# Performance work log

Hardware: AMD Instinct MI355X
Metric: run time of the kernel (lower is better)

## Reference

```python
import jax, jax.numpy as jnp
import numpy as np

HIDDEN = 2048
N_HEADS = 16
N_KV_HEADS = 8
HEAD_DIM = 128
ROTARY_DIM = 32  # int(128 * 0.25), already even
ROPE_THETA = 10000000.0
EPS = 1e-6
BATCH, SEQ = 2, 2048


def _rmsnorm(x, w, eps=EPS):
    # per-head RMSNorm over last dim; weight is zero-init, scale = 1 + w
    r = jax.lax.rsqrt(jnp.mean(x * x, axis=-1, keepdims=True) + eps)
    return x * r * (1.0 + w)


def _rope(x, positions, rotary_dim, theta):
    # x: [b, s, h, rotary_dim]; rotate-halves RoPE
    half = rotary_dim // 2
    inv_freq = 1.0 / (theta ** (jnp.arange(half, dtype=jnp.float32) / half))
    ang = positions.astype(jnp.float32)[:, :, None] * inv_freq  # [b, s, half]
    cos = jnp.cos(ang)[:, :, None, :]
    sin = jnp.sin(ang)[:, :, None, :]
    x1, x2 = x[..., :half], x[..., half:]
    return jnp.concatenate([x1 * cos - x2 * sin, x1 * sin + x2 * cos], axis=-1)


def setup_inputs() -> dict:
    key = jax.random.key(0)
    ks = jax.random.split(key, 8)
    scale = lambda fan_in: 1.0 / np.sqrt(fan_in)
    x = jax.random.normal(ks[0], (BATCH, SEQ, HIDDEN), dtype=jnp.float32)
    Wq = jax.random.normal(ks[1], (HIDDEN, N_HEADS * HEAD_DIM * 2), jnp.float32) * scale(HIDDEN)
    Wk = jax.random.normal(ks[2], (HIDDEN, N_KV_HEADS * HEAD_DIM), jnp.float32) * scale(HIDDEN)
    Wv = jax.random.normal(ks[3], (HIDDEN, N_KV_HEADS * HEAD_DIM), jnp.float32) * scale(HIDDEN)
    Wo = jax.random.normal(ks[4], (N_HEADS * HEAD_DIM, HIDDEN), jnp.float32) * scale(N_HEADS * HEAD_DIM)
    q_norm_w = jax.random.normal(ks[5], (HEAD_DIM,), jnp.float32) * 0.02
    k_norm_w = jax.random.normal(ks[6], (HEAD_DIM,), jnp.float32) * 0.02
    attention_mask = jnp.ones((BATCH, SEQ), dtype=jnp.int32)
    positions = jnp.broadcast_to(jnp.arange(SEQ, dtype=jnp.int32), (BATCH, SEQ))
    return {"x": x, "attention_mask": attention_mask, "positions": positions,
            "Wq": Wq, "Wk": Wk, "Wv": Wv, "Wo": Wo,
            "q_norm_w": q_norm_w, "k_norm_w": k_norm_w}


def reference(x, attention_mask, positions, Wq, Wk, Wv, Wo, q_norm_w, k_norm_w):
    b, s, _ = x.shape
    g = N_HEADS // N_KV_HEADS  # GQA group size

    q_all = jnp.einsum('bsh,ho->bso', x, Wq).reshape(b, s, N_HEADS, HEAD_DIM * 2)
    q, gate = jnp.split(q_all, 2, axis=-1)          # each [b,s,H,D]
    gate = gate.reshape(b, s, N_HEADS * HEAD_DIM)
    q = _rmsnorm(q, q_norm_w)
    k = _rmsnorm(jnp.einsum('bsh,ho->bso', x, Wk).reshape(b, s, N_KV_HEADS, HEAD_DIM), k_norm_w)
    v = jnp.einsum('bsh,ho->bso', x, Wv).reshape(b, s, N_KV_HEADS, HEAD_DIM)

    # partial RoPE on first ROTARY_DIM dims
    q = jnp.concatenate([_rope(q[..., :ROTARY_DIM], positions, ROTARY_DIM, ROPE_THETA), q[..., ROTARY_DIM:]], axis=-1)
    k = jnp.concatenate([_rope(k[..., :ROTARY_DIM], positions, ROTARY_DIM, ROPE_THETA), k[..., ROTARY_DIM:]], axis=-1)

    # grouped-query causal attention
    qg = q.reshape(b, s, N_KV_HEADS, g, HEAD_DIM)
    scores = jnp.einsum('bqhgd,bkhd->bhgqk', qg, k) / jnp.sqrt(jnp.float32(HEAD_DIM))
    causal = jnp.tril(jnp.ones((s, s), dtype=bool))
    key_valid = attention_mask.astype(bool)[:, None, None, None, :]  # [b,1,1,1,k]
    mask = causal[None, None, None, :, :] & key_valid
    scores = jnp.where(mask, scores, jnp.finfo(scores.dtype).min)
    probs = jax.nn.softmax(scores, axis=-1)
    attn = jnp.einsum('bhgqk,bkhd->bqhgd', probs, v).reshape(b, s, N_HEADS * HEAD_DIM)

    attn = attn * jax.nn.sigmoid(gate)
    return jnp.einsum('bso,oh->bsh', attn, Wo)
```

## Files before the change

### kernel.cpp

```cpp
#include <hip/hip_runtime.h>
#include <cstdint>

typedef __bf16  bf16;
typedef __bf16  bf16x8 __attribute__((ext_vector_type(8)));
typedef __bf16  bf16x4 __attribute__((ext_vector_type(4)));
typedef __bf16  bf16x2 __attribute__((ext_vector_type(2)));
typedef float   f32x4  __attribute__((ext_vector_type(4)));
typedef float   f32x16 __attribute__((ext_vector_type(16)));

#define GLOAD_LDS16(g, l) __builtin_amdgcn_global_load_lds( \
    (const __attribute__((address_space(1))) void*)(g),     \
    (__attribute__((address_space(3))) void*)(l), 16, 0, 0)

#define SEQ   2048
#define HID   2048
#define NH    16
#define NKV   8
#define HD    128
#define NQKV  6144
#define MTOT  4096

__device__ __forceinline__ void transw_body(const float* __restrict__ W, bf16* __restrict__ WT,
                                            int N, int n0, int k0, int t) {
    __shared__ float tile[64][65];
    int tn = t & 63, t4 = t >> 6;
    #pragma unroll
    for (int i = 0; i < 16; ++i) {
        int kk = i * 4 + t4;
        tile[kk][tn] = W[(size_t)(k0 + kk) * N + n0 + tn];
    }
    __syncthreads();
    #pragma unroll
    for (int i = 0; i < 16; ++i) {
        int nn = i * 4 + t4;
        WT[(size_t)(n0 + nn) * HID + k0 + tn] = (bf16)tile[tn][nn];
    }
}

__global__ __launch_bounds__(256) void prep_kernel(const float* __restrict__ x, bf16* __restrict__ xb,
                                                   const float* __restrict__ Wq, const float* __restrict__ Wk,
                                                   const float* __restrict__ Wv, const float* __restrict__ Wo,
                                                   bf16* __restrict__ wqkvT, bf16* __restrict__ woT) {
    int bx = blockIdx.x, t = threadIdx.x;
    if (bx < 8192) {
        int i = bx * 256 + t;
        f32x4 v = ((const f32x4*)x)[i];
        bf16x4 o;
        o[0] = (bf16)v[0]; o[1] = (bf16)v[1]; o[2] = (bf16)v[2]; o[3] = (bf16)v[3];
        ((bf16x4*)xb)[i] = o;
    } else if (bx < 8192 + 2048) {
        int idx = bx - 8192;
        transw_body(Wq, wqkvT, 4096, (idx & 63) * 64, (idx >> 6) * 64, t);
    } else if (bx < 8192 + 2048 + 512) {
        int idx = bx - (8192 + 2048);
        transw_body(Wk, wqkvT + (size_t)4096 * HID, 1024, (idx & 15) * 64, (idx >> 4) * 64, t);
    } else if (bx < 8192 + 2048 + 1024) {
        int idx = bx - (8192 + 2048 + 512);
        transw_body(Wv, wqkvT + (size_t)5120 * HID, 1024, (idx & 15) * 64, (idx >> 4) * 64, t);
    } else {
        int idx = bx - (8192 + 2048 + 1024);
        transw_body(Wo, woT, 2048, (idx & 31) * 64, (idx >> 5) * 64, t);
    }
}

template<bool OUT_BF16>
__global__ __launch_bounds__(256) void gemm_bt(const bf16* __restrict__ A, const bf16* __restrict__ Bt,
                                               void* __restrict__ C, int M, int N, int K) {
    __shared__ __align__(16) bf16 As[128 * 64];
    __shared__ __align__(16) bf16 Bs[128 * 64];
    const int tid = threadIdx.x;
    const int wave = tid >> 6, lane = tid & 63;
    const int l31 = lane & 31, half = lane >> 5;
    const int tile_n = blockIdx.x * 128, tile_m = blockIdx.y * 128;
    const int wm = (wave & 1) * 64, wn = (wave >> 1) * 64;
    const int sw = l31 & 7;
    f32x16 acc[2][2] = {};

    for (int k0 = 0; k0 < K; k0 += 64) {
        __syncthreads();
        #pragma unroll
        for (int j = 0; j < 4; ++j) {
            int s = j * 256 + tid;
            int row = s >> 3, c = s & 7;
            int cs = c ^ (row & 7);
            GLOAD_LDS16(A  + (size_t)(tile_m + row) * K + k0 + (cs << 3), As + (size_t)s * 8);
            GLOAD_LDS16(Bt + (size_t)(tile_n + row) * K + k0 + (cs << 3), Bs + (size_t)s * 8);
        }
        __syncthreads();
        #pragma unroll
        for (int ks = 0; ks < 4; ++ks) {
            int ch = ((ks * 2 + half) ^ sw) << 3;
            bf16x8 a0 = *(const bf16x8*)(As + (size_t)(wm + l31) * 64 + ch);
            bf16x8 a1 = *(const bf16x8*)(As + (size_t)(wm + 32 + l31) * 64 + ch);
            bf16x8 b0 = *(const bf16x8*)(Bs + (size_t)(wn + l31) * 64 + ch);
            bf16x8 b1 = *(const bf16x8*)(Bs + (size_t)(wn + 32 + l31) * 64 + ch);
            acc[0][0] = __builtin_amdgcn_mfma_f32_32x32x16_bf16(a0, b0, acc[0][0], 0, 0, 0);
            acc[0][1] = __builtin_amdgcn_mfma_f32_32x32x16_bf16(a0, b1, acc[0][1], 0, 0, 0);
            acc[1][0] = __builtin_amdgcn_mfma_f32_32x32x16_bf16(a1, b0, acc[1][0], 0, 0, 0);
            acc[1][1] = __builtin_amdgcn_mfma_f32_32x32x16_bf16(a1, b1, acc[1][1], 0, 0, 0);
        }
    }
    #pragma unroll
    for (int mt = 0; mt < 2; ++mt)
        #pragma unroll
        for (int nt = 0; nt < 2; ++nt)
            #pragma unroll
            for (int reg = 0; reg < 16; ++reg) {
                int row = tile_m + wm + mt * 32 + (reg & 3) + ((reg >> 2) * 8) + half * 4;
                int col = tile_n + wn + nt * 32 + l31;
                float v = acc[mt][nt][reg];
                if (OUT_BF16) ((bf16*)C)[(size_t)row * N + col] = (bf16)v;
                else          ((float*)C)[(size_t)row * N + col] = v;
            }
}

__global__ __launch_bounds__(256) void post_kernel(const bf16* __restrict__ qkv,
                                                   const float* __restrict__ qnw, const float* __restrict__ knw,
                                                   const int* __restrict__ positions,
                                                   bf16* __restrict__ Qh, bf16* __restrict__ Kh,
                                                   bf16* __restrict__ VT) {
    int bx = blockIdx.x;
    if (bx < 4096) {
        int tk = bx;
        int b = tk >> 11, s = tk & 2047;
        int wave = threadIdx.x >> 6, lane = threadIdx.x & 63;
        int e0 = lane * 2, e1 = e0 + 1;
        float pos = (float)positions[tk];
        const float L = 1.4533435415278355f;
        float a0 = pos * exp2f(-(float)(e0 & 15) * L);
        float a1 = pos * exp2f(-(float)(e1 & 15) * L);
        float cv0 = cosf(a0), sv0 = sinf(a0);
        float cv1 = cosf(a1), sv1 = sinf(a1);
        float qw0 = 1.0f + qnw[e0], qw1 = 1.0f + qnw[e1];
        float kw0 = 1.0f + knw[e0], kw1 = 1.0f + knw[e1];

        #pragma unroll
        for (int i = 0; i < 6; ++i) {
            bool isq = (i < 4);
            int h = wave + (isq ? i : (i - 4)) * 4;
            const bf16* base = qkv + (size_t)tk * NQKV + (isq ? h * 256 : 4096 + h * HD);
            bf16x2 v = *(const bf16x2*)(base + e0);
            float f0 = (float)v[0], f1 = (float)v[1];
            float ssq = f0 * f0 + f1 * f1;
            #pragma unroll
            for (int off = 32; off; off >>= 1) ssq += __shfl_xor(ssq, off);
            float rn = rsqrtf(ssq * (1.0f / 128.0f) + 1e-6f);
            float w0 = isq ? qw0 : kw0, w1 = isq ? qw1 : kw1;
            float x0 = f0 * rn * w0, x1 = f1 * rn * w1;
            float p0 = __shfl_xor(x0, 8), p1 = __shfl_xor(x1, 8);
            float r0 = x0, r1 = x1;
            if (lane < 8)       { r0 = x0 * cv0 - p0 * sv0; r1 = x1 * cv1 - p1 * sv1; }
            else if (lane < 16) { r0 = p0 * sv0 + x0 * cv0; r1 = p1 * sv1 + x1 * cv1; }
            bf16x2 o; o[0] = (bf16)r0; o[1] = (bf16)r1;
            bf16* dst = isq ? (Qh + ((size_t)(b * NH + h) * SEQ + s) * HD)
                            : (Kh + ((size_t)(b * NKV + h) * SEQ + s) * HD);
            *(bf16x2*)(dst + e0) = o;
        }
    } else {
        int idx = bx - 4096;
        int bh = idx >> 5, st = idx & 31;
        int b = bh >> 3, h = bh & 7;
        __shared__ float tile[64][129];
        int t = threadIdx.x;
        const bf16* src = qkv + ((size_t)(b * SEQ) + st * 64) * NQKV + 5120 + h * HD;
        #pragma unroll
        for (int i = 0; i < 32; ++i) {
            int ii = i * 256 + t;
            int tok = ii >> 7, d = ii & 127;
            tile[tok][d] = (float)src[(size_t)tok * NQKV + d];
        }
        __syncthreads();
        bf16* dst = VT + (size_t)(b * NKV + h) * HD * SEQ + st * 64;
        #pragma unroll
        for (int i = 0; i < 32; ++i) {
            int ii = i * 256 + t;
            int d = ii >> 6, sx = ii & 63;
            dst[(size_t)d * SEQ + sx] = (bf16)tile[sx][d];
        }
    }
}

__global__ __launch_bounds__(512, 4) void attn_kernel(const bf16* __restrict__ Qh, const bf16* __restrict__ Kh,
                                                      const bf16* __restrict__ VT, const bf16* __restrict__ qkv,
                                                      const int* __restrict__ amask, bf16* __restrict__ attnb) {
    const int bx = blockIdx.x;
    const int hb = (bx >> 4) & 31;
    const int head = hb & 15, b = hb >> 4;
    int q0 = ((bx & 15) + hb) & 15;
    const int qt = (bx & 256) ? (15 - q0) : q0;
    const int kvh = head >> 1;
    __shared__ __align__(16) bf16 Ks[64 * 128];
    __shared__ __align__(16) bf16 Vs[128 * 64];
    __shared__ __align__(16) bf16 Ps[8 * 16 * 64];
    const int tid = threadIdx.x, wave = tid >> 6, lane = tid & 63;
    const int quad = lane >> 4, cl = lane & 15;

    const bf16* qsrc = Qh + ((size_t)(b * NH + head) * SEQ + qt * 128) * HD;
    bf16x8 aq[4];
    #pragma unroll
    for (int kc = 0; kc < 4; ++kc)
        aq[kc] = *(const bf16x8*)(qsrc + (size_t)(wave * 16 + cl) * HD + kc * 32 + quad * 8);

    float lstate[4] = {0.0f, 0.0f, 0.0f, 0.0f};
    f32x4 oacc[8] = {};
    const int qrow_glob = qt * 128 + wave * 16 + quad * 4;
    const float scale = 0.08838834764831845f * 1.4426950408889634f;
    const float M = 20.0f;
    const int kmax = 2 * qt + 1;

    for (int kt = 0; kt <= kmax; ++kt) {
        __syncthreads();
        const bf16* ksrc = Kh + ((size_t)(b * NKV + kvh) * SEQ + kt * 64) * HD;
        const bf16* vsrc = VT + (size_t)(b * NKV + kvh) * HD * SEQ + kt * 64;
        #pragma unroll
        for (int j = 0; j < 2; ++j) {
            int s = j * 512 + tid;
            int rK = s >> 4, cK = s & 15;
            GLOAD_LDS16(ksrc + (size_t)rK * HD + ((cK ^ (rK & 15)) << 3), Ks + (size_t)s * 8);
            int dV = s >> 3, cV = s & 7;
            GLOAD_LDS16(vsrc + (size_t)dV * SEQ + ((cV ^ (dV & 7)) << 3), Vs + (size_t)s * 8);
        }
        __syncthreads();

        f32x4 sc[4] = {};
        #pragma unroll
        for (int nt = 0; nt < 4; ++nt)
            #pragma unroll
            for (int kc = 0; kc < 4; ++kc) {
                bf16x8 bk = *(const bf16x8*)(Ks + (size_t)(nt * 16 + cl) * 128 + (((kc * 4 + quad) ^ cl) << 3));
                sc[nt] = __builtin_amdgcn_mfma_f32_16x16x32_bf16(aq[kc], bk, sc[nt], 0, 0, 0);
            }

        #pragma unroll
        for (int nt = 0; nt < 4; ++nt) {
            int kcol = kt * 64 + nt * 16 + cl;
            bool cok = (amask[b * SEQ + kcol] != 0);
            #pragma unroll
            for (int r = 0; r < 4; ++r) {
                bool ok = cok && (kcol <= qrow_glob + r);
                float p = ok ? exp2f(sc[nt][r] * scale - M) : 0.0f;
                lstate[r] += p;
                Ps[wave * 1024 + (quad * 4 + r) * 64 + ((nt * 16 + cl) ^ (quad << 4))] = (bf16)p;
            }
        }

        bf16x8 ap[2];
        #pragma unroll
        for (int c = 0; c < 2; ++c)
            ap[c] = *(const bf16x8*)(Ps + wave * 1024 + cl * 64 + ((c * 32 + quad * 8) ^ ((cl >> 2) << 4)));
        #pragma unroll
        for (int n2 = 0; n2 < 8; ++n2)
            #pragma unroll
            for (int c = 0; c < 2; ++c) {
                bf16x8 bv = *(const bf16x8*)(Vs + (size_t)(n2 * 16 + cl) * 64 + (((c * 4 + quad) ^ (cl & 7)) << 3));
                oacc[n2] = __builtin_amdgcn_mfma_f32_16x16x32_bf16(ap[c], bv, oacc[n2], 0, 0, 0);
            }
    }

    #pragma unroll
    for (int r = 0; r < 4; ++r) {
        #pragma unroll
        for (int off = 8; off; off >>= 1) lstate[r] += __shfl_xor(lstate[r], off);
        int srow = qt * 128 + wave * 16 + quad * 4 + r;
        float linv = 1.0f / lstate[r];
        #pragma unroll
        for (int n2 = 0; n2 < 8; ++n2) {
            int d = n2 * 16 + cl;
            float g = (float)qkv[(size_t)(b * SEQ + srow) * NQKV + head * 256 + 128 + d];
            float sig = 1.0f / (1.0f + __expf(-g));
            float v = oacc[n2][r] * linv * sig;
            attnb[(size_t)(b * SEQ + srow) * HID + head * HD + d] = (bf16)v;
        }
    }
}

extern "C" void kernel_launch(void* const* d_in, const int* in_sizes, int n_in,
                              void* d_out, int out_size, void* d_ws, size_t ws_size,
                              hipStream_t stream) {
    const float* x        = (const float*)d_in[0];
    const int*   amask    = (const int*)d_in[1];
    const int*   positions= (const int*)d_in[2];
    const float* Wq       = (const float*)d_in[3];
    const float* Wk       = (const float*)d_in[4];
    const float* Wv       = (const float*)d_in[5];
    const float* Wo       = (const float*)d_in[6];
    const float* qnw      = (const float*)d_in[7];
    const float* knw      = (const float*)d_in[8];
    float* out = (float*)d_out;
    char* ws = (char*)d_ws;

    bf16* xb    = (bf16*)(ws);
    bf16* wqkvT = (bf16*)(ws + 16777216);
    bf16* woT   = (bf16*)(ws + 41943040);
    bf16* qkv   = (bf16*)(ws + 50331648);
    bf16* Qh    = (bf16*)(ws + 100663296);
    bf16* Kh    = (bf16*)(ws + 117440512);
    bf16* VT    = (bf16*)(ws + 125829120);
    bf16* attnb = (bf16*)(ws + 134217728);

    prep_kernel<<<12288, 256, 0, stream>>>(x, xb, Wq, Wk, Wv, Wo, wqkvT, woT);
    gemm_bt<true><<<dim3(48, 32), 256, 0, stream>>>(xb, wqkvT, qkv, MTOT, NQKV, HID);
    post_kernel<<<4608, 256, 0, stream>>>(qkv, qnw, knw, positions, Qh, Kh, VT);
    attn_kernel<<<512, 512, 0, stream>>>(Qh, Kh, VT, qkv, amask, attnb);
    gemm_bt<false><<<dim3(16, 32), 256, 0, stream>>>(attnb, woT, out, MTOT, HID, HID);

    (void)in_sizes; (void)n_in; (void)out_size; (void)ws_size;
}
```

Before: 396.4 us.

## Restructure attention to 32x32 MFMA tiles with 128-key blocks and 4 waves

Rewrites the attention kernel to use 32x32x16 bf16 MFMA instead of 16x16x32. Each of 4 waves now owns 32 query rows, and K/V tiles grow to 128 keys. Fewer synchronisations and LDS loads per FLOP are intended, and fully masked sub-blocks on the diagonal are skipped for the lower waves. In exchange it uses more LDS (about 80 KB per block) and more registers per thread, which reduces occupancy.

```diff
diff --git a/kernel.cpp b/kernel.cpp
--- a/kernel.cpp
+++ b/kernel.cpp
@@ -180,98 +180,115 @@
     }
 }
 
-__global__ __launch_bounds__(512, 4) void attn_kernel(const bf16* __restrict__ Qh, const bf16* __restrict__ Kh,
-                                                      const bf16* __restrict__ VT, const bf16* __restrict__ qkv,
-                                                      const int* __restrict__ amask, bf16* __restrict__ attnb) {
+__global__ __launch_bounds__(256) void attn_kernel(const bf16* __restrict__ Qh, const bf16* __restrict__ Kh,
+                                                   const bf16* __restrict__ VT, const bf16* __restrict__ qkv,
+                                                   const int* __restrict__ amask, bf16* __restrict__ attnb) {
     const int bx = blockIdx.x;
     const int hb = (bx >> 4) & 31;
     const int head = hb & 15, b = hb >> 4;
     int q0 = ((bx & 15) + hb) & 15;
     const int qt = (bx & 256) ? (15 - q0) : q0;
     const int kvh = head >> 1;
-    __shared__ __align__(16) bf16 Ks[64 * 128];
-    __shared__ __align__(16) bf16 Vs[128 * 64];
-    __shared__ __align__(16) bf16 Ps[8 * 16 * 64];
+    __shared__ __align__(16) bf16 Ks[128 * 128];
+    __shared__ __align__(16) bf16 Vs[128 * 128];
+    __shared__ __align__(16) bf16 Ps[4 * 32 * 64];
     const int tid = threadIdx.x, wave = tid >> 6, lane = tid & 63;
-    const int quad = lane >> 4, cl = lane & 15;
-
-    const bf16* qsrc = Qh + ((size_t)(b * NH + head) * SEQ + qt * 128) * HD;
-    bf16x8 aq[4];
-    #pragma unroll
-    for (int kc = 0; kc < 4; ++kc)
-        aq[kc] = *(const bf16x8*)(qsrc + (size_t)(wave * 16 + cl) * HD + kc * 32 + quad * 8);
-
-    float lstate[4] = {0.0f, 0.0f, 0.0f, 0.0f};
-    f32x4 oacc[8] = {};
-    const int qrow_glob = qt * 128 + wave * 16 + quad * 4;
+    const int l31 = lane & 31, half = lane >> 5;
+
+    const bf16* qsrc = Qh + ((size_t)(b * NH + head) * SEQ + qt * 128 + wave * 32 + l31) * HD;
+    bf16x8 aq[8];
+    #pragma unroll
+    for (int kk = 0; kk < 8; ++kk)
+        aq[kk] = *(const bf16x8*)(qsrc + kk * 16 + half * 8);
+
+    float lstate[16];
+    #pragma unroll
+    for (int r = 0; r < 16; ++r) lstate[r] = 0.0f;
+    f32x16 oacc[4] = {};
     const float scale = 0.08838834764831845f * 1.4426950408889634f;
-    const float M = 20.0f;
-    const int kmax = 2 * qt + 1;
-
-    for (int kt = 0; kt <= kmax; ++kt) {
-        __syncthreads();
-        const bf16* ksrc = Kh + ((size_t)(b * NKV + kvh) * SEQ + kt * 64) * HD;
-        const bf16* vsrc = VT + (size_t)(b * NKV + kvh) * HD * SEQ + kt * 64;
-        #pragma unroll
-        for (int j = 0; j < 2; ++j) {
-            int s = j * 512 + tid;
-            int rK = s >> 4, cK = s & 15;
-            GLOAD_LDS16(ksrc + (size_t)rK * HD + ((cK ^ (rK & 15)) << 3), Ks + (size_t)s * 8);
-            int dV = s >> 3, cV = s & 7;
-            GLOAD_LDS16(vsrc + (size_t)dV * SEQ + ((cV ^ (dV & 7)) << 3), Vs + (size_t)s * 8);
-        }
-        __syncthreads();
-
-        f32x4 sc[4] = {};
-        #pragma unroll
-        for (int nt = 0; nt < 4; ++nt)
-            #pragma unroll
-            for (int kc = 0; kc < 4; ++kc) {
-                bf16x8 bk = *(const bf16x8*)(Ks + (size_t)(nt * 16 + cl) * 128 + (((kc * 4 + quad) ^ cl) << 3));
-                sc[nt] = __builtin_amdgcn_mfma_f32_16x16x32_bf16(aq[kc], bk, sc[nt], 0, 0, 0);
+    const float Mx = 20.0f;
+
+    for (int kt = 0; kt <= qt; ++kt) {
+        __syncthreads();
+        const bf16* ksrc = Kh + ((size_t)(b * NKV + kvh) * SEQ + kt * 128) * HD;
+        const bf16* vsrc = VT + (size_t)(b * NKV + kvh) * HD * SEQ + kt * 128;
+        #pragma unroll
+        for (int j = 0; j < 8; ++j) {
+            int s = j * 256 + tid;
+            int r = s >> 4, c = s & 15;
+            int cs = (c ^ (r & 15)) << 3;
+            GLOAD_LDS16(ksrc + (size_t)r * HD + cs, Ks + (size_t)s * 8);
+            GLOAD_LDS16(vsrc + (size_t)r * SEQ + cs, Vs + (size_t)s * 8);
+        }
+        __syncthreads();
+
+        #pragma unroll
+        for (int sub = 0; sub < 2; ++sub) {
+            if (kt == qt && sub == 1 && wave < 2) break;
+
+            f32x16 sc[2] = {};
+            #pragma unroll
+            for (int tile = 0; tile < 2; ++tile)
+                #pragma unroll
+                for (int kk = 0; kk < 8; ++kk) {
+                    int srow = sub * 64 + tile * 32 + l31;
+                    int ch = ((kk * 2 + half) ^ (l31 & 15)) << 3;
+                    bf16x8 bk = *(const bf16x8*)(Ks + (size_t)srow * 128 + ch);
+                    sc[tile] = __builtin_amdgcn_mfma_f32_32x32x16_bf16(aq[kk], bk, sc[tile], 0, 0, 0);
+                }
+
+            #pragma unroll
+            for (int tile = 0; tile < 2; ++tile) {
+                int kcol = kt * 128 + sub * 64 + tile * 32 + l31;
+                bool cok = (amask[b * SEQ + kcol] != 0);
+                #pragma unroll
+                for (int reg = 0; reg < 16; ++reg) {
+                    int row = (reg & 3) + ((reg >> 2) * 8) + half * 4;
+                    int qrow = qt * 128 + wave * 32 + row;
+                    bool ok = cok && (kcol <= qrow);
+                    float p = ok ? exp2f(sc[tile][reg] * scale - Mx) : 0.0f;
+                    lstate[reg] += p;
+                    int col = tile * 32 + l31;
+                    int chn = (col >> 3) ^ (row & 7);
+                    Ps[wave * 2048 + row * 64 + chn * 8 + (col & 7)] = (bf16)p;
+                }
             }
 
-        #pragma unroll
-        for (int nt = 0; nt < 4; ++nt) {
-            int kcol = kt * 64 + nt * 16 + cl;
-            bool cok = (amask[b * SEQ + kcol] != 0);
-            #pragma unroll
-            for (int r = 0; r < 4; ++r) {
-                bool ok = cok && (kcol <= qrow_glob + r);
-                float p = ok ? exp2f(sc[nt][r] * scale - M) : 0.0f;
-                lstate[r] += p;
-                Ps[wave * 1024 + (quad * 4 + r) * 64 + ((nt * 16 + cl) ^ (quad << 4))] = (bf16)p;
-            }
-        }
-
-        bf16x8 ap[2];
-        #pragma unroll
-        for (int c = 0; c < 2; ++c)
-            ap[c] = *(const bf16x8*)(Ps + wave * 1024 + cl * 64 + ((c * 32 + quad * 8) ^ ((cl >> 2) << 4)));
-        #pragma unroll
-        for (int n2 = 0; n2 < 8; ++n2)
-            #pragma unroll
-            for (int c = 0; c < 2; ++c) {
-                bf16x8 bv = *(const bf16x8*)(Vs + (size_t)(n2 * 16 + cl) * 64 + (((c * 4 + quad) ^ (cl & 7)) << 3));
-                oacc[n2] = __builtin_amdgcn_mfma_f32_16x16x32_bf16(ap[c], bv, oacc[n2], 0, 0, 0);
-            }
-    }
-
-    #pragma unroll
-    for (int r = 0; r < 4; ++r) {
-        #pragma unroll
-        for (int off = 8; off; off >>= 1) lstate[r] += __shfl_xor(lstate[r], off);
-        int srow = qt * 128 + wave * 16 + quad * 4 + r;
-        float linv = 1.0f / lstate[r];
-        #pragma unroll
-        for (int n2 = 0; n2 < 8; ++n2) {
-            int d = n2 * 16 + cl;
+            bf16x8 ap[4];
+            #pragma unroll
+            for (int kc = 0; kc < 4; ++kc)
+                ap[kc] = *(const bf16x8*)(Ps + wave * 2048 + l31 * 64 + (((kc * 2 + half) ^ (l31 & 7)) << 3));
+            #pragma unroll
+            for (int nt = 0; nt < 4; ++nt)
+                #pragma unroll
+                for (int kc = 0; kc < 4; ++kc) {
+                    int d = nt * 32 + l31;
+                    int ch = ((sub * 8 + kc * 2 + half) ^ (l31 & 15)) << 3;
+                    bf16x8 bv = *(const bf16x8*)(Vs + (size_t)d * 128 + ch);
+                    oacc[nt] = __builtin_amdgcn_mfma_f32_32x32x16_bf16(ap[kc], bv, oacc[nt], 0, 0, 0);
+                }
+        }
+    }
+
+    #pragma unroll
+    for (int reg = 0; reg < 16; ++reg) {
+        float l = lstate[reg];
+        #pragma unroll
+        for (int off = 16; off; off >>= 1) l += __shfl_xor(l, off);
+        lstate[reg] = 1.0f / l;
+    }
+    #pragma unroll
+    for (int nt = 0; nt < 4; ++nt)
+        #pragma unroll
+        for (int reg = 0; reg < 16; ++reg) {
+            int row = (reg & 3) + ((reg >> 2) * 8) + half * 4;
+            int srow = qt * 128 + wave * 32 + row;
+            int d = nt * 32 + l31;
             float g = (float)qkv[(size_t)(b * SEQ + srow) * NQKV + head * 256 + 128 + d];
             float sig = 1.0f / (1.0f + __expf(-g));
-            float v = oacc[n2][r] * linv * sig;
+            float v = oacc[nt][reg] * lstate[reg] * sig;
             attnb[(size_t)(b * SEQ + srow) * HID + head * HD + d] = (bf16)v;
         }
-    }
 }
 
 extern "C" void kernel_launch(void* const* d_in, const int* in_sizes, int n_in,
@@ -301,7 +318,7 @@
     prep_kernel<<<12288, 256, 0, stream>>>(x, xb, Wq, Wk, Wv, Wo, wqkvT, woT);
     gemm_bt<true><<<dim3(48, 32), 256, 0, stream>>>(xb, wqkvT, qkv, MTOT, NQKV, HID);
     post_kernel<<<4608, 256, 0, stream>>>(qkv, qnw, knw, positions, Qh, Kh, VT);
-    attn_kernel<<<512, 512, 0, stream>>>(Qh, Kh, VT, qkv, amask, attnb);
+    attn_kernel<<<512, 256, 0, stream>>>(Qh, Kh, VT, qkv, amask, attnb);
     gemm_bt<false><<<dim3(16, 32), 256, 0, stream>>>(attnb, woT, out, MTOT, HID, HID);
 
     (void)in_sizes; (void)n_in; (void)out_size; (void)ws_size;
```

Result: slower. 516.4 us (+30.3%).

## Halve attention block to 4 waves, each handling two 16-row query fragments

Applied to the files above, without the earlier changes.

The attention kernel now launches 256 threads per block instead of 512. Each wave computes two 16-row query fragments (rows wave*16 and 64+wave*16), so every K and V fragment read from LDS is reused for two MFMAs. On the final diagonal key tile the first fragment's MFMAs and softmax are skipped, because those rows are fully masked. This trades more registers per wave (double accumulators and Q fragments) and fewer waves for latency hiding against lower LDS read traffic and less redundant work.

```diff
diff --git a/kernel.cpp b/kernel.cpp
--- a/kernel.cpp
+++ b/kernel.cpp
@@ -180,9 +180,9 @@
     }
 }
 
-__global__ __launch_bounds__(512, 4) void attn_kernel(const bf16* __restrict__ Qh, const bf16* __restrict__ Kh,
-                                                      const bf16* __restrict__ VT, const bf16* __restrict__ qkv,
-                                                      const int* __restrict__ amask, bf16* __restrict__ attnb) {
+__global__ __launch_bounds__(256) void attn_kernel(const bf16* __restrict__ Qh, const bf16* __restrict__ Kh,
+                                                   const bf16* __restrict__ VT, const bf16* __restrict__ qkv,
+                                                   const int* __restrict__ amask, bf16* __restrict__ attnb) {
     const int bx = blockIdx.x;
     const int hb = (bx >> 4) & 31;
     const int head = hb & 15, b = hb >> 4;
@@ -196,16 +196,17 @@
     const int quad = lane >> 4, cl = lane & 15;
 
     const bf16* qsrc = Qh + ((size_t)(b * NH + head) * SEQ + qt * 128) * HD;
-    bf16x8 aq[4];
-    #pragma unroll
-    for (int kc = 0; kc < 4; ++kc)
-        aq[kc] = *(const bf16x8*)(qsrc + (size_t)(wave * 16 + cl) * HD + kc * 32 + quad * 8);
-
-    float lstate[4] = {0.0f, 0.0f, 0.0f, 0.0f};
-    f32x4 oacc[8] = {};
-    const int qrow_glob = qt * 128 + wave * 16 + quad * 4;
+    bf16x8 aq[2][4];
+    #pragma unroll
+    for (int rf = 0; rf < 2; ++rf)
+        #pragma unroll
+        for (int kc = 0; kc < 4; ++kc)
+            aq[rf][kc] = *(const bf16x8*)(qsrc + (size_t)(rf * 64 + wave * 16 + cl) * HD + kc * 32 + quad * 8);
+
+    float lstate[2][4] = {};
+    f32x4 oacc[2][8] = {};
     const float scale = 0.08838834764831845f * 1.4426950408889634f;
-    const float M = 20.0f;
+    const float Mx = 20.0f;
     const int kmax = 2 * qt + 1;
 
     for (int kt = 0; kt <= kmax; ++kt) {
@@ -213,8 +214,8 @@
         const bf16* ksrc = Kh + ((size_t)(b * NKV + kvh) * SEQ + kt * 64) * HD;
         const bf16* vsrc = VT + (size_t)(b * NKV + kvh) * HD * SEQ + kt * 64;
         #pragma unroll
-        for (int j = 0; j < 2; ++j) {
-            int s = j * 512 + tid;
+        for (int j = 0; j < 4; ++j) {
+            int s = j * 256 + tid;
             int rK = s >> 4, cK = s & 15;
             GLOAD_LDS16(ksrc + (size_t)rK * HD + ((cK ^ (rK & 15)) << 3), Ks + (size_t)s * 8);
             int dV = s >> 3, cV = s & 7;
@@ -222,56 +223,70 @@
         }
         __syncthreads();
 
-        f32x4 sc[4] = {};
+        const bool act0 = (kt != kmax);
+
+        f32x4 sc[2][4] = {};
         #pragma unroll
         for (int nt = 0; nt < 4; ++nt)
             #pragma unroll
             for (int kc = 0; kc < 4; ++kc) {
                 bf16x8 bk = *(const bf16x8*)(Ks + (size_t)(nt * 16 + cl) * 128 + (((kc * 4 + quad) ^ cl) << 3));
-                sc[nt] = __builtin_amdgcn_mfma_f32_16x16x32_bf16(aq[kc], bk, sc[nt], 0, 0, 0);
-            }
-
-        #pragma unroll
-        for (int nt = 0; nt < 4; ++nt) {
-            int kcol = kt * 64 + nt * 16 + cl;
-            bool cok = (amask[b * SEQ + kcol] != 0);
-            #pragma unroll
-            for (int r = 0; r < 4; ++r) {
-                bool ok = cok && (kcol <= qrow_glob + r);
-                float p = ok ? exp2f(sc[nt][r] * scale - M) : 0.0f;
-                lstate[r] += p;
-                Ps[wave * 1024 + (quad * 4 + r) * 64 + ((nt * 16 + cl) ^ (quad << 4))] = (bf16)p;
-            }
-        }
-
-        bf16x8 ap[2];
-        #pragma unroll
-        for (int c = 0; c < 2; ++c)
-            ap[c] = *(const bf16x8*)(Ps + wave * 1024 + cl * 64 + ((c * 32 + quad * 8) ^ ((cl >> 2) << 4)));
+                if (act0) sc[0][nt] = __builtin_amdgcn_mfma_f32_16x16x32_bf16(aq[0][kc], bk, sc[0][nt], 0, 0, 0);
+                sc[1][nt] = __builtin_amdgcn_mfma_f32_16x16x32_bf16(aq[1][kc], bk, sc[1][nt], 0, 0, 0);
+            }
+
+        #pragma unroll
+        for (int rf = 0; rf < 2; ++rf) {
+            if (rf == 0 && !act0) continue;
+            const int qrow = qt * 128 + rf * 64 + wave * 16 + quad * 4;
+            #pragma unroll
+            for (int nt = 0; nt < 4; ++nt) {
+                int kcol = kt * 64 + nt * 16 + cl;
+                bool cok = (amask[b * SEQ + kcol] != 0);
+                #pragma unroll
+                for (int r = 0; r < 4; ++r) {
+                    bool ok = cok && (kcol <= qrow + r);
+                    float p = ok ? exp2f(sc[rf][nt][r] * scale - Mx) : 0.0f;
+                    lstate[rf][r] += p;
+                    Ps[(wave * 2 + rf) * 1024 + (quad * 4 + r) * 64 + ((nt * 16 + cl) ^ (quad << 4))] = (bf16)p;
+                }
+            }
+        }
+
+        bf16x8 ap[2][2];
+        #pragma unroll
+        for (int rf = 0; rf < 2; ++rf)
+            #pragma unroll
+            for (int c = 0; c < 2; ++c)
+                ap[rf][c] = *(const bf16x8*)(Ps + (wave * 2 + rf) * 1024 + cl * 64 + ((c * 32 + quad * 8) ^ ((cl >> 2) << 4)));
         #pragma unroll
         for (int n2 = 0; n2 < 8; ++n2)
             #pragma unroll
             for (int c = 0; c < 2; ++c) {
                 bf16x8 bv = *(const bf16x8*)(Vs + (size_t)(n2 * 16 + cl) * 64 + (((c * 4 + quad) ^ (cl & 7)) << 3));
-                oacc[n2] = __builtin_amdgcn_mfma_f32_16x16x32_bf16(ap[c], bv, oacc[n2], 0, 0, 0);
-            }
-    }
-
-    #pragma unroll
-    for (int r = 0; r < 4; ++r) {
-        #pragma unroll
-        for (int off = 8; off; off >>= 1) lstate[r] += __shfl_xor(lstate[r], off);
-        int srow = qt * 128 + wave * 16 + quad * 4 + r;
-        float linv = 1.0f / lstate[r];
-        #pragma unroll
-        for (int n2 = 0; n2 < 8; ++n2) {
-            int d = n2 * 16 + cl;
-            float g = (float)qkv[(size_t)(b * SEQ + srow) * NQKV + head * 256 + 128 + d];
-            float sig = 1.0f / (1.0f + __expf(-g));
-            float v = oacc[n2][r] * linv * sig;
-            attnb[(size_t)(b * SEQ + srow) * HID + head * HD + d] = (bf16)v;
-        }
-    }
+                if (act0) oacc[0][n2] = __builtin_amdgcn_mfma_f32_16x16x32_bf16(ap[0][c], bv, oacc[0][n2], 0, 0, 0);
+                oacc[1][n2] = __builtin_amdgcn_mfma_f32_16x16x32_bf16(ap[1][c], bv, oacc[1][n2], 0, 0, 0);
+            }
+    }
+
+    #pragma unroll
+    for (int rf = 0; rf < 2; ++rf)
+        #pragma unroll
+        for (int r = 0; r < 4; ++r) {
+            float l = lstate[rf][r];
+            #pragma unroll
+            for (int off = 8; off; off >>= 1) l += __shfl_xor(l, off);
+            float linv = 1.0f / l;
+            int srow = qt * 128 + rf * 64 + wave * 16 + quad * 4 + r;
+            #pragma unroll
+            for (int n2 = 0; n2 < 8; ++n2) {
+                int d = n2 * 16 + cl;
+                float g = (float)qkv[(size_t)(b * SEQ + srow) * NQKV + head * 256 + 128 + d];
+                float sig = 1.0f / (1.0f + __expf(-g));
+                float v = oacc[rf][n2][r] * linv * sig;
+                attnb[(size_t)(b * SEQ + srow) * HID + head * HD + d] = (bf16)v;
+            }
+        }
 }
 
 extern "C" void kernel_launch(void* const* d_in, const int* in_sizes, int n_in,
@@ -301,7 +316,7 @@
     prep_kernel<<<12288, 256, 0, stream>>>(x, xb, Wq, Wk, Wv, Wo, wqkvT, woT);
     gemm_bt<true><<<dim3(48, 32), 256, 0, stream>>>(xb, wqkvT, qkv, MTOT, NQKV, HID);
     post_kernel<<<4608, 256, 0, stream>>>(qkv, qnw, knw, positions, Qh, Kh, VT);
-    attn_kernel<<<512, 512, 0, stream>>>(Qh, Kh, VT, qkv, amask, attnb);
+    attn_kernel<<<512, 256, 0, stream>>>(Qh, Kh, VT, qkv, amask, attnb);
     gemm_bt<false><<<dim3(16, 32), 256, 0, stream>>>(attnb, woT, out, MTOT, HID, HID);
 
     (void)in_sizes; (void)n_in; (void)out_size; (void)ws_size;
```

Result: slower. 450.9 us (+13.8%).
